# Kernel optimization log

Measured on AMD Instinct MI355X. Metric: run time of the kernel, lower is better.

Reference implementation:

```python
import jax, jax.numpy as jnp
import numpy as np

B, N, D, K = 32, 4096, 256, 128


def setup_inputs() -> dict:
    key = jax.random.key(0)
    k1, k2, k3 = jax.random.split(key, 3)
    x = jax.random.normal(k1, (B, N, D), dtype=jnp.float32)
    # 'orthogonal' init proxy: unit-variance-ish codewords
    codewords = jax.random.normal(k2, (K, D), dtype=jnp.float32) / np.float32(np.sqrt(D))
    # keras 'uniform' initializer default range (-0.05, 0.05)
    scale = jax.random.uniform(k3, (K,), dtype=jnp.float32, minval=-0.05, maxval=0.05)
    return {"x": x, "codewords": codewords, "scale": scale}


def reference(x, codewords, scale):
    """Deep-TEN Encoding layer.

    scaledL2: w_ik = S_k * ||x_i - c_k||^2   (expanded, avoids (B,N,K,D) residuals)
    weights : W = softmax_k(w_ik)
    aggregate: E_k = sum_i W_ik * (x_i - c_k)
    """
    x2 = jnp.sum(x * x, axis=-1)                    # (B, N)
    c2 = jnp.sum(codewords * codewords, axis=-1)    # (K,)
    xc = jnp.einsum('bnd,kd->bnk', x, codewords)    # (B, N, K)
    sl2 = scale * (x2[..., None] - 2.0 * xc + c2)   # (B, N, K)
    W = jax.nn.softmax(sl2, axis=-1)                # softmax over codewords K
    # E_k = sum_i W_ik x_i - (sum_i W_ik) c_k
    E = jnp.einsum('bnk,bnd->bkd', W, x) - jnp.sum(W, axis=1)[..., None] * codewords
    return E  # (B, K, D)
```

## Files before the change

### kernel.cpp

```cpp
#include <hip/hip_runtime.h>

#define DEV __device__ __forceinline__

typedef __attribute__((ext_vector_type(8))) short bf16x8;
typedef __attribute__((ext_vector_type(4))) float f32x4;

constexpr int Nn = 4096, Dd = 256, Kk = 128;
constexpr int SEGS = 32;
constexpr int CH2  = 8;
constexpr int NCH  = Nn / CH2;
constexpr int NSTEP = 64;

DEV unsigned short f2bf(float f) {
  unsigned int u = __builtin_bit_cast(unsigned int, f);
  u += 0x7FFFu + ((u >> 16) & 1u);
  return (unsigned short)(u >> 16);
}
DEV float bf2f(unsigned short h) {
  unsigned int u = (unsigned int)h << 16;
  return __builtin_bit_cast(float, u);
}

DEV unsigned lds2(unsigned d, unsigned nbyte) {
  unsigned hh = (d & 7u) ^ ((d >> 4) & 7u) ^ (((d >> 7) & 1u) << 1);
  return d * 128u + (nbyte ^ (hh << 4));
}

DEV unsigned ldsc(unsigned row, unsigned byteInRow) {
  return row * 512u + (byteInRow ^ ((row & 7u) << 4));
}

__global__ void enc_prep(const float* __restrict__ cw, const float* __restrict__ sc,
                         unsigned short* __restrict__ cbf, float2* __restrict__ tab) {
  int k = blockIdx.x, l = threadIdx.x;
  float4 u = *(const float4*)(cw + k * Dd + l * 4);
  float s2 = u.x * u.x + u.y * u.y + u.z * u.z + u.w * u.w;
  #pragma unroll
  for (int o = 1; o < 64; o <<= 1) s2 += __shfl_xor(s2, o);
  unsigned short* dst = cbf + k * Dd + l * 4;
  dst[0] = f2bf(u.x); dst[1] = f2bf(u.y); dst[2] = f2bf(u.z); dst[3] = f2bf(u.w);
  if (l == 0) { float s = sc[k]; tab[k] = make_float2(s * s2, 2.0f * s); }
}

__global__ __launch_bounds__(512, 1) void enc_w(
    const float* __restrict__ x, const unsigned short* __restrict__ cbf,
    const float2* __restrict__ tab, unsigned short* __restrict__ Wt) {
  __shared__ __align__(16) char cL[65536];
  __shared__ float2 tabL[Kk];
  const int tid = threadIdx.x;
  const int w  = tid >> 6;
  const int l  = tid & 63;
  const int g  = l >> 4;
  const int ln = l & 15;

  {
    const int r = tid >> 2, part = tid & 3;
    const char* src = (const char*)cbf + r * 512 + part * 128;
    #pragma unroll
    for (int j = 0; j < 8; ++j) {
      float4 v = *(const float4*)(src + j * 16);
      *(float4*)(cL + ldsc((unsigned)r, (unsigned)(part * 128 + j * 16))) = v;
    }
  }
  if (tid < Kk) tabL[tid] = tab[tid];
  __syncthreads();

  const int b   = blockIdx.x >> 5;
  const int seg = blockIdx.x & 31;
  const int nrow = seg * 128 + w * 16 + ln;
  const float* xrow = x + ((size_t)b * Nn + nrow) * Dd;

  f32x4 s1[8];
  const f32x4 zero4 = {0.f, 0.f, 0.f, 0.f};
  #pragma unroll
  for (int f = 0; f < 8; ++f) s1[f] = zero4;
  float x2p = 0.f;

  float4 pu[8][2];
  #pragma unroll
  for (int p = 0; p < 8; ++p) {
    pu[p][0] = *(const float4*)(xrow + p * 32 + g * 8);
    pu[p][1] = *(const float4*)(xrow + p * 32 + g * 8 + 4);
  }

  #pragma unroll
  for (int ks = 0; ks < 8; ++ks) {
    float4 u0 = pu[ks][0], u1 = pu[ks][1];
    x2p += u0.x*u0.x + u0.y*u0.y + u0.z*u0.z + u0.w*u0.w
         + u1.x*u1.x + u1.y*u1.y + u1.z*u1.z + u1.w*u1.w;
    bf16x8 xv;
    xv[0] = (short)f2bf(u0.x); xv[1] = (short)f2bf(u0.y);
    xv[2] = (short)f2bf(u0.z); xv[3] = (short)f2bf(u0.w);
    xv[4] = (short)f2bf(u1.x); xv[5] = (short)f2bf(u1.y);
    xv[6] = (short)f2bf(u1.z); xv[7] = (short)f2bf(u1.w);
    const unsigned colb = (unsigned)(ks * 64 + g * 16);
    #pragma unroll
    for (int f = 0; f < 8; ++f) {
      bf16x8 a = *(const bf16x8*)(cL + ldsc((unsigned)(f * 16 + ln), colb));
      s1[f] = __builtin_amdgcn_mfma_f32_16x16x32_bf16(a, xv, s1[f], 0, 0, 0);
    }
  }

  x2p += __shfl_xor(x2p, 16); x2p += __shfl_xor(x2p, 32);
  const float hx2 = 0.5f * x2p;
  float ssum = 0.f;
  #pragma unroll
  for (int f = 0; f < 8; ++f) {
    #pragma unroll
    for (int r = 0; r < 4; ++r) {
      const float2 ab = tabL[f * 16 + g * 4 + r];
      const float ev = __expf(ab.x + ab.y * (hx2 - s1[f][r]));
      s1[f][r] = ev;
      ssum += ev;
    }
  }
  ssum += __shfl_xor(ssum, 16); ssum += __shfl_xor(ssum, 32);
  const float rinv = 1.0f / ssum;

  unsigned short* wb = Wt + (size_t)b * Kk * Nn + nrow;
  #pragma unroll
  for (int f = 0; f < 8; ++f) {
    #pragma unroll
    for (int r = 0; r < 4; ++r) {
      const int cwi = f * 16 + g * 4 + r;
      wb[(size_t)cwi * Nn] = f2bf(s1[f][r] * rinv);
    }
  }
}

template<int PM>
__global__ __launch_bounds__(1024) void enc_e(
    const float* __restrict__ x, const unsigned short* __restrict__ Wt,
    const float* __restrict__ cwf, float* __restrict__ Ep, float* __restrict__ out) {
  __shared__ __align__(16) char xs[2 * 32768];
  __shared__ float wsL[Kk];

  const int tid = threadIdx.x;
  const int w  = tid >> 6;
  const int l  = tid & 63;
  const int g  = l >> 4;
  const int ln = l & 15;
  const int wr = w >> 2, wc = w & 3;
  const int b  = blockIdx.x >> 3, ch = blockIdx.x & 7;

  const float* xb = x + ((size_t)b * Nn + ch * NCH) * Dd;
  const unsigned short* Wb = Wt + (size_t)b * Kk * Nn + ch * NCH;

  const int srow = w * 4 + g;
  const int sd0  = ln * 16;

  f32x4 acc[2][4];
  const f32x4 zero4 = {0.f, 0.f, 0.f, 0.f};
  #pragma unroll
  for (int mi = 0; mi < 2; ++mi)
    #pragma unroll
    for (int ni = 0; ni < 4; ++ni) acc[mi][ni] = zero4;
  float ws0 = 0.f, ws1 = 0.f;

  {
    const float* p = xb + (size_t)srow * Dd + sd0;
    float4 u0 = *(const float4*)(p + 0), u1 = *(const float4*)(p + 4);
    float4 u2 = *(const float4*)(p + 8), u3 = *(const float4*)(p + 12);
    const float uu[16] = {u0.x,u0.y,u0.z,u0.w, u1.x,u1.y,u1.z,u1.w,
                          u2.x,u2.y,u2.z,u2.w, u3.x,u3.y,u3.z,u3.w};
    #pragma unroll
    for (int j = 0; j < 16; ++j)
      *(unsigned short*)(xs + lds2((unsigned)(sd0 + j), (unsigned)(srow * 2))) = f2bf(uu[j]);
  }
  bf16x8 wf[2][2];
  #pragma unroll
  for (int ks2 = 0; ks2 < 2; ++ks2)
    #pragma unroll
    for (int mi = 0; mi < 2; ++mi)
      wf[ks2][mi] = *(const bf16x8*)(Wb + (size_t)(wr * 32 + mi * 16 + ln) * Nn
                                        + ks2 * 32 + g * 8);
  __syncthreads();

  int cur = 0;
  for (int s = 0; s < CH2; ++s) {
    float4 n0, n1, n2, n3;
    bf16x8 wn[2][2];
    if (s + 1 < CH2) {
      const float* p = xb + (size_t)((s + 1) * NSTEP + srow) * Dd + sd0;
      n0 = *(const float4*)(p + 0); n1 = *(const float4*)(p + 4);
      n2 = *(const float4*)(p + 8); n3 = *(const float4*)(p + 12);
      #pragma unroll
      for (int ks2 = 0; ks2 < 2; ++ks2)
        #pragma unroll
        for (int mi = 0; mi < 2; ++mi)
          wn[ks2][mi] = *(const bf16x8*)(Wb + (size_t)(wr * 32 + mi * 16 + ln) * Nn
                                            + (s + 1) * NSTEP + ks2 * 32 + g * 8);
    }

    const char* xcur = xs + (cur << 15);
    #pragma unroll
    for (int ks2 = 0; ks2 < 2; ++ks2) {
      bf16x8 bg[4];
      #pragma unroll
      for (int ni = 0; ni < 4; ++ni)
        bg[ni] = *(const bf16x8*)(xcur + lds2((unsigned)(wc * 64 + ni * 16 + ln),
                                              (unsigned)((ks2 * 32 + g * 8) * 2)));
      #pragma unroll
      for (int mi = 0; mi < 2; ++mi) {
        float wsp = 0.f;
        #pragma unroll
        for (int j = 0; j < 8; ++j) wsp += bf2f((unsigned short)wf[ks2][mi][j]);
        if (mi == 0) ws0 += wsp; else ws1 += wsp;
        #pragma unroll
        for (int ni = 0; ni < 4; ++ni)
          acc[mi][ni] = __builtin_amdgcn_mfma_f32_16x16x32_bf16(wf[ks2][mi], bg[ni], acc[mi][ni], 0, 0, 0);
      }
    }

    if (s + 1 < CH2) {
      char* xn = xs + ((cur ^ 1) << 15);
      const float uu[16] = {n0.x,n0.y,n0.z,n0.w, n1.x,n1.y,n1.z,n1.w,
                            n2.x,n2.y,n2.z,n2.w, n3.x,n3.y,n3.z,n3.w};
      #pragma unroll
      for (int j = 0; j < 16; ++j)
        *(unsigned short*)(xn + lds2((unsigned)(sd0 + j), (unsigned)(srow * 2))) = f2bf(uu[j]);
      #pragma unroll
      for (int ks2 = 0; ks2 < 2; ++ks2)
        #pragma unroll
        for (int mi = 0; mi < 2; ++mi)
          wf[ks2][mi] = wn[ks2][mi];
    }
    __syncthreads();
    cur ^= 1;
  }

  ws0 += __shfl_xor(ws0, 16); ws0 += __shfl_xor(ws0, 32);
  ws1 += __shfl_xor(ws1, 16); ws1 += __shfl_xor(ws1, 32);
  if (wc == 0 && l < 16) {
    wsL[wr * 32 + l]      = ws0;
    wsL[wr * 32 + 16 + l] = ws1;
  }
  __syncthreads();

  #pragma unroll
  for (int mi = 0; mi < 2; ++mi) {
    #pragma unroll
    for (int r = 0; r < 4; ++r) {
      const int k = wr * 32 + mi * 16 + g * 4 + r;
      const float wsv = wsL[k];
      #pragma unroll
      for (int ni = 0; ni < 4; ++ni) {
        const int d = wc * 64 + ni * 16 + ln;
        const float v = acc[mi][ni][r] - wsv * cwf[k * Dd + d];
        if (PM == 0) {
          Ep[(size_t)blockIdx.x * (Kk * Dd) + k * Dd + d] = v;
        } else {
          atomicAdd(out + (size_t)b * (Kk * Dd) + k * Dd + d, v);
        }
      }
    }
  }
}

__global__ __launch_bounds__(256, 1) void enc_reduce_f32(
    const float* __restrict__ Ep, float* __restrict__ out) {
  const size_t i = ((size_t)blockIdx.x * 256 + threadIdx.x) * 16;
  const int b   = (int)(i / (Kk * Dd));
  const int rem = (int)(i % (Kk * Dd));
  const float* p = Ep + (size_t)b * CH2 * (Kk * Dd) + rem;
  float sx[16];
  #pragma unroll
  for (int j = 0; j < 16; ++j) sx[j] = 0.f;
  #pragma unroll
  for (int c = 0; c < CH2; ++c) {
    const float4* q = (const float4*)(p + (size_t)c * (Kk * Dd));
    float4 v0 = q[0], v1 = q[1], v2 = q[2], v3 = q[3];
    sx[0] += v0.x; sx[1] += v0.y; sx[2]  += v0.z; sx[3]  += v0.w;
    sx[4] += v1.x; sx[5] += v1.y; sx[6]  += v1.z; sx[7]  += v1.w;
    sx[8] += v2.x; sx[9] += v2.y; sx[10] += v2.z; sx[11] += v2.w;
    sx[12] += v3.x; sx[13] += v3.y; sx[14] += v3.z; sx[15] += v3.w;
  }
  float4* o = (float4*)(out + i);
  o[0] = make_float4(sx[0], sx[1], sx[2], sx[3]);
  o[1] = make_float4(sx[4], sx[5], sx[6], sx[7]);
  o[2] = make_float4(sx[8], sx[9], sx[10], sx[11]);
  o[3] = make_float4(sx[12], sx[13], sx[14], sx[15]);
}

extern "C" void kernel_launch(void* const* d_in, const int* in_sizes, int n_in,
                              void* d_out, int out_size, void* d_ws, size_t ws_size,
                              hipStream_t stream) {
  const float* x  = (const float*)d_in[0];
  const float* cw = (const float*)d_in[1];
  const float* sc = (const float*)d_in[2];
  float* out = (float*)d_out;

  unsigned short* cbf = (unsigned short*)d_ws;
  float2* tab = (float2*)((char*)d_ws + 65536);
  unsigned short* Wt = (unsigned short*)((char*)d_ws + 66560);
  float* Ep = (float*)((char*)d_ws + 66560 + (size_t)32 * Kk * Nn * 2);
  const size_t KD = (size_t)Kk * Dd;
  const size_t needFull = 66560 + (size_t)32 * Kk * Nn * 2 + (size_t)32 * CH2 * KD * 4;
  const size_t needAtm  = 66560 + (size_t)32 * Kk * Nn * 2;

  enc_prep<<<dim3(Kk), dim3(64), 0, stream>>>(cw, sc, cbf, tab);
  enc_w<<<dim3(32 * SEGS), dim3(512), 0, stream>>>(x, cbf, tab, Wt);

  if (ws_size >= needFull) {
    enc_e<0><<<dim3(32 * CH2), dim3(1024), 0, stream>>>(x, Wt, cw, Ep, nullptr);
    enc_reduce_f32<<<dim3(256), dim3(256), 0, stream>>>(Ep, out);
  } else if (ws_size >= needAtm) {
    hipMemsetAsync(d_out, 0, (size_t)out_size * sizeof(float), stream);
    enc_e<2><<<dim3(32 * CH2), dim3(1024), 0, stream>>>(x, Wt, cw, nullptr, out);
  }
}
```

Baseline: 99.33 us.

## Stage softmax weights through LDS for coalesced stores; store partials in bf16

Result: faster. 94.56 us (-4.8%).

```diff
diff --git a/kernel.cpp b/kernel.cpp
--- a/kernel.cpp
+++ b/kernel.cpp
@@ -28,6 +28,11 @@
 
 DEV unsigned ldsc(unsigned row, unsigned byteInRow) {
   return row * 512u + (byteInRow ^ ((row & 7u) << 4));
+}
+
+DEV unsigned ldsw(unsigned k, unsigned nbyte) {
+  unsigned h = (k & 7u) ^ (((k >> 3) & 1u) << 1);
+  return k * 256u + (nbyte ^ (h << 4));
 }
 
 __global__ void enc_prep(const float* __restrict__ cw, const float* __restrict__ sc,
@@ -117,13 +122,25 @@
   ssum += __shfl_xor(ssum, 16); ssum += __shfl_xor(ssum, 32);
   const float rinv = 1.0f / ssum;
 
-  unsigned short* wb = Wt + (size_t)b * Kk * Nn + nrow;
+  __syncthreads();
   #pragma unroll
   for (int f = 0; f < 8; ++f) {
     #pragma unroll
     for (int r = 0; r < 4; ++r) {
       const int cwi = f * 16 + g * 4 + r;
-      wb[(size_t)cwi * Nn] = f2bf(s1[f][r] * rinv);
+      *(unsigned short*)(cL + ldsw((unsigned)cwi, (unsigned)((w * 16 + ln) * 2)))
+          = f2bf(s1[f][r] * rinv);
+    }
+  }
+  __syncthreads();
+  {
+    char* wq = (char*)(Wt + (size_t)b * Kk * Nn + seg * 128);
+    #pragma unroll
+    for (int j = 0; j < 4; ++j) {
+      const unsigned o = (unsigned)tid * 16u + (unsigned)j * 8192u;
+      const unsigned k = o >> 8, nb = o & 255u;
+      float4 v = *(const float4*)(cL + ldsw(k, nb));
+      *(float4*)(wq + (size_t)k * (Nn * 2) + nb) = v;
     }
   }
 }
@@ -131,7 +148,8 @@
 template<int PM>
 __global__ __launch_bounds__(1024) void enc_e(
     const float* __restrict__ x, const unsigned short* __restrict__ Wt,
-    const float* __restrict__ cwf, float* __restrict__ Ep, float* __restrict__ out) {
+    const float* __restrict__ cwf, unsigned short* __restrict__ Ep,
+    float* __restrict__ out) {
   __shared__ __align__(16) char xs[2 * 32768];
   __shared__ float wsL[Kk];
 
@@ -248,7 +266,7 @@
         const int d = wc * 64 + ni * 16 + ln;
         const float v = acc[mi][ni][r] - wsv * cwf[k * Dd + d];
         if (PM == 0) {
-          Ep[(size_t)blockIdx.x * (Kk * Dd) + k * Dd + d] = v;
+          Ep[(size_t)blockIdx.x * (Kk * Dd) + k * Dd + d] = f2bf(v);
         } else {
           atomicAdd(out + (size_t)b * (Kk * Dd) + k * Dd + d, v);
         }
@@ -257,23 +275,23 @@
   }
 }
 
-__global__ __launch_bounds__(256, 1) void enc_reduce_f32(
-    const float* __restrict__ Ep, float* __restrict__ out) {
+__global__ __launch_bounds__(256, 1) void enc_reduce_b16(
+    const unsigned short* __restrict__ Ep, float* __restrict__ out) {
   const size_t i = ((size_t)blockIdx.x * 256 + threadIdx.x) * 16;
   const int b   = (int)(i / (Kk * Dd));
   const int rem = (int)(i % (Kk * Dd));
-  const float* p = Ep + (size_t)b * CH2 * (Kk * Dd) + rem;
+  const unsigned short* p = Ep + (size_t)b * CH2 * (Kk * Dd) + rem;
   float sx[16];
   #pragma unroll
   for (int j = 0; j < 16; ++j) sx[j] = 0.f;
   #pragma unroll
   for (int c = 0; c < CH2; ++c) {
-    const float4* q = (const float4*)(p + (size_t)c * (Kk * Dd));
-    float4 v0 = q[0], v1 = q[1], v2 = q[2], v3 = q[3];
-    sx[0] += v0.x; sx[1] += v0.y; sx[2]  += v0.z; sx[3]  += v0.w;
-    sx[4] += v1.x; sx[5] += v1.y; sx[6]  += v1.z; sx[7]  += v1.w;
-    sx[8] += v2.x; sx[9] += v2.y; sx[10] += v2.z; sx[11] += v2.w;
-    sx[12] += v3.x; sx[13] += v3.y; sx[14] += v3.z; sx[15] += v3.w;
+    const ushort4* q = (const ushort4*)(p + (size_t)c * (Kk * Dd));
+    ushort4 v0 = q[0], v1 = q[1], v2 = q[2], v3 = q[3];
+    sx[0]  += bf2f(v0.x); sx[1]  += bf2f(v0.y); sx[2]  += bf2f(v0.z); sx[3]  += bf2f(v0.w);
+    sx[4]  += bf2f(v1.x); sx[5]  += bf2f(v1.y); sx[6]  += bf2f(v1.z); sx[7]  += bf2f(v1.w);
+    sx[8]  += bf2f(v2.x); sx[9]  += bf2f(v2.y); sx[10] += bf2f(v2.z); sx[11] += bf2f(v2.w);
+    sx[12] += bf2f(v3.x); sx[13] += bf2f(v3.y); sx[14] += bf2f(v3.z); sx[15] += bf2f(v3.w);
   }
   float4* o = (float4*)(out + i);
   o[0] = make_float4(sx[0], sx[1], sx[2], sx[3]);
@@ -293,9 +311,9 @@
   unsigned short* cbf = (unsigned short*)d_ws;
   float2* tab = (float2*)((char*)d_ws + 65536);
   unsigned short* Wt = (unsigned short*)((char*)d_ws + 66560);
-  float* Ep = (float*)((char*)d_ws + 66560 + (size_t)32 * Kk * Nn * 2);
+  unsigned short* Ep = (unsigned short*)((char*)d_ws + 66560 + (size_t)32 * Kk * Nn * 2);
   const size_t KD = (size_t)Kk * Dd;
-  const size_t needFull = 66560 + (size_t)32 * Kk * Nn * 2 + (size_t)32 * CH2 * KD * 4;
+  const size_t needFull = 66560 + (size_t)32 * Kk * Nn * 2 + (size_t)32 * CH2 * KD * 2;
   const size_t needAtm  = 66560 + (size_t)32 * Kk * Nn * 2;
 
   enc_prep<<<dim3(Kk), dim3(64), 0, stream>>>(cw, sc, cbf, tab);
@@ -303,7 +321,7 @@
 
   if (ws_size >= needFull) {
     enc_e<0><<<dim3(32 * CH2), dim3(1024), 0, stream>>>(x, Wt, cw, Ep, nullptr);
-    enc_reduce_f32<<<dim3(256), dim3(256), 0, stream>>>(Ep, out);
+    enc_reduce_b16<<<dim3(256), dim3(256), 0, stream>>>(Ep, out);
   } else if (ws_size >= needAtm) {
     hipMemsetAsync(d_out, 0, (size_t)out_size * sizeof(float), stream);
     enc_e<2><<<dim3(32 * CH2), dim3(1024), 0, stream>>>(x, Wt, cw, nullptr, out);
```
